# Performance work log

Hardware: AMD Instinct MI355X
Metric: run time of the kernel (lower is better)

## Reference

```python
import jax, jax.numpy as jnp
import numpy as np

G = 64      # norm_groups
T = 5       # Newton-Schulz iterations
EPS = 1e-5


def setup_inputs() -> dict:
    key = jax.random.key(0)
    weight = jax.random.normal(key, (2048, 18432), dtype=jnp.float32)
    return {"weight": weight}


def reference(weight):
    out_ch = weight.shape[0]
    # Z: [G, c, d] with c = out_ch // G, d = prod(rest)
    Z = weight.reshape(G, out_ch // G, -1)
    Zc = Z - jnp.mean(Z, axis=-1, keepdims=True)
    # S = Zc @ Zc^T : [G, c, c]
    S = jnp.einsum('gcd,ged->gce', Zc, Zc)
    c = S.shape[-1]
    eye = jnp.eye(c, dtype=S.dtype)
    S = S + EPS * eye
    # Frobenius norm per group, keepdim -> [G,1,1]
    norm_S = jnp.sqrt(jnp.sum(S * S, axis=(1, 2), keepdims=True))
    S = S / norm_S
    # Newton-Schulz: B_{t+1} = 1.5*B_t - 0.5 * B_t^3 @ S
    B = jnp.broadcast_to(eye, S.shape)
    for _ in range(T):
        B3 = jnp.matmul(jnp.matmul(B, B), B)
        B = 1.5 * B - 0.5 * jnp.matmul(B3, S)
    W = jnp.matmul(B, Zc) / jnp.sqrt(norm_S)
    return W.reshape(weight.shape)
```

## Files before the change

kernel.cpp:

```cpp
#include <hip/hip_runtime.h>

#define G 64
#define C 32
#define D 18432
#define NCH 16
#define TD (D / NCH)
#define NST (TD / 128)
#define EPS 1e-5f
#define NS_ITERS 5

typedef __attribute__((ext_vector_type(8))) short short8v;
typedef __attribute__((ext_vector_type(4))) float float4v;

__device__ __forceinline__ void split3(float x, unsigned short& h1,
                                       unsigned short& h2, unsigned short& h3) {
    unsigned int u = __float_as_uint(x);
    unsigned int m1 = u & 0xffff0000u;
    float r1 = x - __uint_as_float(m1);
    unsigned int u2 = __float_as_uint(r1);
    unsigned int m2 = u2 & 0xffff0000u;
    float r2 = r1 - __uint_as_float(m2);
    h1 = (unsigned short)(m1 >> 16);
    h2 = (unsigned short)(m2 >> 16);
    h3 = (unsigned short)(__float_as_uint(r2) >> 16);
}

__device__ __forceinline__ void split8(const float4& v0, const float4& v1,
                                       short8v& p1, short8v& p2, short8v& p3,
                                       float& rs) {
    float x[8] = {v0.x, v0.y, v0.z, v0.w, v1.x, v1.y, v1.z, v1.w};
#pragma unroll
    for (int j = 0; j < 8; ++j) {
        unsigned short h1, h2, h3;
        rs += x[j];
        split3(x[j], h1, h2, h3);
        p1[j] = (short)h1; p2[j] = (short)h2; p3[j] = (short)h3;
    }
}

#define MM6(T, A0, A1, A2, B0, B1, B2)                                        \
    T = __builtin_amdgcn_mfma_f32_16x16x32_bf16(A0, B0, T, 0, 0, 0);          \
    T = __builtin_amdgcn_mfma_f32_16x16x32_bf16(A0, B1, T, 0, 0, 0);          \
    T = __builtin_amdgcn_mfma_f32_16x16x32_bf16(A1, B0, T, 0, 0, 0);          \
    T = __builtin_amdgcn_mfma_f32_16x16x32_bf16(A1, B1, T, 0, 0, 0);          \
    T = __builtin_amdgcn_mfma_f32_16x16x32_bf16(A0, B2, T, 0, 0, 0);          \
    T = __builtin_amdgcn_mfma_f32_16x16x32_bf16(A2, B0, T, 0, 0, 0);

__global__ __launch_bounds__(256) void k1_gram(const float* __restrict__ W,
                                               float* __restrict__ psum,
                                               float* __restrict__ prow) {
    __shared__ float red[4 * 1056 + 4 * C];

    const int ch   = blockIdx.x;
    const int g    = blockIdx.y;
    const int bid  = g * NCH + ch;
    const int tid  = threadIdx.x;
    const int lane = tid & 63;
    const int wave = tid >> 6;

    const int rbase = lane & 15;
    const int koff  = (lane >> 4) * 8;

    const float* Zg = W + (size_t)g * C * D + (size_t)ch * TD;
    const float* p0 = Zg + (size_t)rbase * D + wave * 32 + koff;
    const float* p1 = p0 + (size_t)16 * D;

    float4v acc00 = (float4v)0.f, acc01 = (float4v)0.f;
    float4v acc10 = (float4v)0.f, acc11 = (float4v)0.f;
    float rs0 = 0.f, rs1 = 0.f;

    float4 c00 = *(const float4*)(p0);
    float4 c01 = *(const float4*)(p0 + 4);
    float4 c10 = *(const float4*)(p1);
    float4 c11 = *(const float4*)(p1 + 4);

#pragma unroll 1
    for (int st = 0; st < NST; ++st) {
        float4 n00, n01, n10, n11;
        if (st + 1 < NST) {
            const float* q0 = p0 + (st + 1) * 128;
            const float* q1 = p1 + (st + 1) * 128;
            n00 = *(const float4*)(q0);
            n01 = *(const float4*)(q0 + 4);
            n10 = *(const float4*)(q1);
            n11 = *(const float4*)(q1 + 4);
        }
        short8v fa0, fa1, fa2, fb0, fb1, fb2;
        split8(c00, c01, fa0, fa1, fa2, rs0);
        split8(c10, c11, fb0, fb1, fb2, rs1);

        MM6(acc00, fa0, fa1, fa2, fa0, fa1, fa2)
        MM6(acc01, fa0, fa1, fa2, fb0, fb1, fb2)
        MM6(acc10, fb0, fb1, fb2, fa0, fa1, fa2)
        MM6(acc11, fb0, fb1, fb2, fb0, fb1, fb2)

        c00 = n00; c01 = n01; c10 = n10; c11 = n11;
    }

    rs0 += __shfl_xor(rs0, 16, 64); rs0 += __shfl_xor(rs0, 32, 64);
    rs1 += __shfl_xor(rs1, 16, 64); rs1 += __shfl_xor(rs1, 32, 64);
    if (lane < 16) {
        red[4224 + wave * C + lane]      = rs0;
        red[4224 + wave * C + 16 + lane] = rs1;
    }

    {
        const int rq  = (lane >> 4) << 2;
        const int cl  = lane & 15;
        float* base = red + wave * 1056;
#pragma unroll
        for (int j = 0; j < 4; ++j) {
            base[(rq + j) * 33 + cl]            = acc00[j];
            base[(rq + j) * 33 + 16 + cl]       = acc01[j];
            base[(16 + rq + j) * 33 + cl]       = acc10[j];
            base[(16 + rq + j) * 33 + 16 + cl]  = acc11[j];
        }
    }
    __syncthreads();

#pragma unroll
    for (int k = 0; k < 4; ++k) {
        int el = tid + 256 * k;
        int row = el >> 5, col = el & 31;
        int o = row * 33 + col;
        float sv = red[o] + red[1056 + o] + red[2112 + o] + red[3168 + o];
        psum[(size_t)bid * (C * C) + el] = sv;
    }
    if (tid < C) {
        float s = red[4224 + tid] + red[4224 + C + tid] +
                  red[4224 + 2 * C + tid] + red[4224 + 3 * C + tid];
        prow[(size_t)bid * C + tid] = s;
    }
}

__global__ __launch_bounds__(256) void k2_ns(const float* __restrict__ psum,
                                             const float* __restrict__ prow,
                                             float* __restrict__ MT,
                                             float* __restrict__ vout) {
    __shared__ float S[C][C + 1];
    __shared__ float B[C][C + 1];
    __shared__ float T1[C][C + 1];
    __shared__ float T2[C][C + 1];
    __shared__ float mean[C];
    __shared__ float redw[4];
    __shared__ float normsh;

    const int g   = blockIdx.x;
    const int tid = threadIdx.x;
    const int e   = tid & 31;
    const int cbq = tid >> 5;

    float selt[4];
#pragma unroll
    for (int k = 0; k < 4; ++k) {
        int el = tid + 256 * k;
        float s = 0.f;
#pragma unroll
        for (int ch = 0; ch < NCH; ++ch)
            s += psum[((size_t)g * NCH + ch) * (C * C) + el];
        selt[k] = s;
    }
    if (tid < C) {
        float s = 0.f;
#pragma unroll
        for (int ch = 0; ch < NCH; ++ch)
            s += prow[((size_t)g * NCH + ch) * C + tid];
        mean[tid] = s / (float)D;
    }
    __syncthreads();

    float ss = 0.f;
#pragma unroll
    for (int k = 0; k < 4; ++k) {
        int el = tid + 256 * k;
        int c = el >> 5;
        float sv = selt[k] - (float)D * mean[c] * mean[e];
        if (c == e) sv += EPS;
        S[c][e] = sv;
        ss = fmaf(sv, sv, ss);
    }
#pragma unroll
    for (int off = 32; off >= 1; off >>= 1) ss += __shfl_xor(ss, off, 64);
    if ((tid & 63) == 0) redw[tid >> 6] = ss;
    __syncthreads();
    if (tid == 0) normsh = sqrtf(redw[0] + redw[1] + redw[2] + redw[3]);
    __syncthreads();
    const float inv_norm = 1.0f / normsh;
#pragma unroll
    for (int k = 0; k < 4; ++k) {
        int c = cbq + 8 * k;
        S[c][e] *= inv_norm;
        B[c][e] = (c == e) ? 1.f : 0.f;
    }
    __syncthreads();

    for (int it = 0; it < NS_ITERS; ++it) {
#pragma unroll
        for (int k = 0; k < 4; ++k) {
            int c = cbq + 8 * k;
            float s = 0.f;
            for (int kk = 0; kk < C; ++kk)
                s = fmaf(B[c][kk], B[kk][e], s);
            T1[c][e] = s;
        }
        __syncthreads();
#pragma unroll
        for (int k = 0; k < 4; ++k) {
            int c = cbq + 8 * k;
            float s = 0.f;
            for (int kk = 0; kk < C; ++kk)
                s = fmaf(T1[c][kk], B[kk][e], s);
            T2[c][e] = s;
        }
        __syncthreads();
        float pv[4];
#pragma unroll
        for (int k = 0; k < 4; ++k) {
            int c = cbq + 8 * k;
            float s = 0.f;
            for (int kk = 0; kk < C; ++kk)
                s = fmaf(T2[c][kk], S[kk][e], s);
            pv[k] = s;
        }
#pragma unroll
        for (int k = 0; k < 4; ++k) {
            int c = cbq + 8 * k;
            B[c][e] = 1.5f * B[c][e] - 0.5f * pv[k];
        }
        __syncthreads();
    }

    const float invs = 1.0f / sqrtf(normsh);
#pragma unroll
    for (int k = 0; k < 4; ++k) {
        int c = cbq + 8 * k;
        MT[(size_t)g * (C * C) + e * C + c] = B[c][e] * invs;
    }
    if (tid < C) {
        float s = 0.f;
        for (int ee = 0; ee < C; ++ee)
            s = fmaf(B[tid][ee] * invs, mean[ee], s);
        vout[(size_t)g * C + tid] = s;
    }
}

__global__ __launch_bounds__(256) void k3_apply(const float* __restrict__ W,
                                                const float* __restrict__ MT,
                                                const float* __restrict__ vv,
                                                float* __restrict__ out) {
    const int bpg = D / 1024;
    const int g   = blockIdx.x / bpg;
    const int cbk = blockIdx.x % bpg;
    const int d0  = cbk * 1024 + (int)threadIdx.x * 4;
    const float* Zg = W + (size_t)g * C * D + d0;
    const float* Mg = MT + (size_t)g * (C * C);

    float4 acc[C];
#pragma unroll
    for (int r = 0; r < C; ++r) acc[r] = make_float4(0.f, 0.f, 0.f, 0.f);

#pragma unroll 4
    for (int e = 0; e < C; ++e) {
        float4 z = *(const float4*)(Zg + (size_t)e * D);
#pragma unroll
        for (int r = 0; r < C; ++r) {
            float m = Mg[e * C + r];
            acc[r].x = fmaf(m, z.x, acc[r].x);
            acc[r].y = fmaf(m, z.y, acc[r].y);
            acc[r].z = fmaf(m, z.z, acc[r].z);
            acc[r].w = fmaf(m, z.w, acc[r].w);
        }
    }

    float* Og = out + (size_t)g * C * D + d0;
#pragma unroll
    for (int r = 0; r < C; ++r) {
        float vr = vv[g * C + r];
        float4 o = make_float4(acc[r].x - vr, acc[r].y - vr,
                               acc[r].z - vr, acc[r].w - vr);
        *(float4*)(Og + (size_t)r * D) = o;
    }
}

extern "C" void kernel_launch(void* const* d_in, const int* in_sizes, int n_in,
                              void* d_out, int out_size, void* d_ws, size_t ws_size,
                              hipStream_t stream) {
    const float* w = (const float*)d_in[0];
    float* out = (float*)d_out;

    float* psum = (float*)d_ws;
    float* prow = psum + (size_t)(G * NCH) * (C * C);
    float* MT   = prow + (size_t)(G * NCH) * C;
    float* vv   = MT   + (size_t)G * (C * C);

    k1_gram<<<dim3(NCH, G), 256, 0, stream>>>(w, psum, prow);
    k2_ns  <<<G,            256, 0, stream>>>(psum, prow, MT, vv);
    k3_apply<<<G * (D / 1024), 256, 0, stream>>>(w, MT, vv, out);
}
```

Baseline: 95.11 us.

## Fuse gram, Newton-Schulz and apply into one cooperative kernel with grid sync

Replaces the three-kernel pipeline with a single cooperative kernel of 256 blocks of 512 threads, four blocks per group. Each block computes a partial Gram over a quarter of the columns, then a grid-wide sync follows. Every block redundantly runs the Newton-Schulz iteration for its group and applies the result to its own column quarter. This removes two kernel launches and the serialized small k2 launch, and may keep W warm in cache, at the cost of a grid barrier, redundant NS work, and far fewer blocks (256) for the memory-bound apply phase. The old three-kernel path remains as a fallback if the workspace is too small or the cooperative launch fails.

After: 186.0 us. 95.6% more time.

```diff
diff --git a/kernel.cpp b/kernel.cpp
--- a/kernel.cpp
+++ b/kernel.cpp
@@ -1,13 +1,18 @@
 #include <hip/hip_runtime.h>
+#include <hip/hip_cooperative_groups.h>
+
+namespace cg = cooperative_groups;
 
 #define G 64
 #define C 32
 #define D 18432
+#define QCOLS 4608
+#define NSTEP (QCOLS / 256)
+#define EPS 1e-5f
+#define NS_ITERS 5
 #define NCH 16
 #define TD (D / NCH)
 #define NST (TD / 128)
-#define EPS 1e-5f
-#define NS_ITERS 5
 
 typedef __attribute__((ext_vector_type(8))) short short8v;
 typedef __attribute__((ext_vector_type(4))) float float4v;
@@ -46,34 +51,263 @@
     T = __builtin_amdgcn_mfma_f32_16x16x32_bf16(A0, B2, T, 0, 0, 0);          \
     T = __builtin_amdgcn_mfma_f32_16x16x32_bf16(A2, B0, T, 0, 0, 0);
 
+__global__ __launch_bounds__(512, 2) void fused_all(const float* __restrict__ W,
+                                                    float* __restrict__ psum,
+                                                    float* __restrict__ prow,
+                                                    float* __restrict__ mtb,
+                                                    float* __restrict__ vvb,
+                                                    float* __restrict__ out) {
+    __shared__ __align__(16) float red[8704];
+    __shared__ float mean[C];
+    __shared__ float redw[8];
+    __shared__ float normsh;
+
+    const int b    = blockIdx.x;
+    const int g    = b >> 2;
+    const int q    = b & 3;
+    const int tid  = threadIdx.x;
+    const int lane = tid & 63;
+    const int wave = tid >> 6;
+
+    {
+        const int rbase = lane & 15;
+        const int koff  = (lane >> 4) * 8;
+        const float* Zg = W + (size_t)g * C * D + (size_t)q * QCOLS;
+        const float* p0 = Zg + (size_t)rbase * D + wave * 32 + koff;
+        const float* p1 = p0 + (size_t)16 * D;
+
+        float4v acc00 = (float4v)0.f, acc01 = (float4v)0.f;
+        float4v acc10 = (float4v)0.f, acc11 = (float4v)0.f;
+        float rs0 = 0.f, rs1 = 0.f;
+
+        float4 c00 = *(const float4*)(p0);
+        float4 c01 = *(const float4*)(p0 + 4);
+        float4 c10 = *(const float4*)(p1);
+        float4 c11 = *(const float4*)(p1 + 4);
+
+#pragma unroll 1
+        for (int st = 0; st < NSTEP; ++st) {
+            float4 n00, n01, n10, n11;
+            if (st + 1 < NSTEP) {
+                const float* q0 = p0 + (st + 1) * 256;
+                const float* q1 = p1 + (st + 1) * 256;
+                n00 = *(const float4*)(q0);
+                n01 = *(const float4*)(q0 + 4);
+                n10 = *(const float4*)(q1);
+                n11 = *(const float4*)(q1 + 4);
+            }
+            short8v fa0, fa1, fa2, fb0, fb1, fb2;
+            split8(c00, c01, fa0, fa1, fa2, rs0);
+            split8(c10, c11, fb0, fb1, fb2, rs1);
+
+            MM6(acc00, fa0, fa1, fa2, fa0, fa1, fa2)
+            MM6(acc01, fa0, fa1, fa2, fb0, fb1, fb2)
+            MM6(acc10, fb0, fb1, fb2, fa0, fa1, fa2)
+            MM6(acc11, fb0, fb1, fb2, fb0, fb1, fb2)
+
+            c00 = n00; c01 = n01; c10 = n10; c11 = n11;
+        }
+
+        rs0 += __shfl_xor(rs0, 16, 64); rs0 += __shfl_xor(rs0, 32, 64);
+        rs1 += __shfl_xor(rs1, 16, 64); rs1 += __shfl_xor(rs1, 32, 64);
+        if (lane < 16) {
+            red[8448 + wave * 32 + lane]      = rs0;
+            red[8448 + wave * 32 + 16 + lane] = rs1;
+        }
+        {
+            const int rq = (lane >> 4) << 2;
+            const int cl = lane & 15;
+            float* base = red + wave * 1056;
+#pragma unroll
+            for (int j = 0; j < 4; ++j) {
+                base[(rq + j) * 33 + cl]           = acc00[j];
+                base[(rq + j) * 33 + 16 + cl]      = acc01[j];
+                base[(16 + rq + j) * 33 + cl]      = acc10[j];
+                base[(16 + rq + j) * 33 + 16 + cl] = acc11[j];
+            }
+        }
+        __syncthreads();
+#pragma unroll
+        for (int k = 0; k < 2; ++k) {
+            int el  = tid + 512 * k;
+            int row = el >> 5, col = el & 31;
+            int o   = row * 33 + col;
+            float sv = 0.f;
+#pragma unroll
+            for (int wv = 0; wv < 8; ++wv) sv += red[wv * 1056 + o];
+            psum[(size_t)b * 1024 + el] = sv;
+        }
+        if (tid < C) {
+            float s = 0.f;
+#pragma unroll
+            for (int wv = 0; wv < 8; ++wv) s += red[8448 + wv * 32 + tid];
+            prow[(size_t)b * 32 + tid] = s;
+        }
+    }
+
+    __threadfence();
+    cg::this_grid().sync();
+
+    {
+        const int e  = tid & 31;
+        const int cb = tid >> 5;
+        float* Sm  = red;
+        float* Bm  = red + 1056;
+        float* T1m = red + 2112;
+        float* T2m = red + 3168;
+
+        float selt0 = 0.f, selt1 = 0.f;
+#pragma unroll
+        for (int q2 = 0; q2 < 4; ++q2) {
+            const float* ps = psum + (size_t)(g * 4 + q2) * 1024;
+            selt0 += ps[tid];
+            selt1 += ps[tid + 512];
+        }
+        if (tid < C) {
+            float s = 0.f;
+#pragma unroll
+            for (int q2 = 0; q2 < 4; ++q2) s += prow[(size_t)(g * 4 + q2) * 32 + tid];
+            mean[tid] = s / (float)D;
+        }
+        __syncthreads();
+
+        float ss = 0.f;
+        {
+            int c = cb;
+            float sv = selt0 - (float)D * mean[c] * mean[e];
+            if (c == e) sv += EPS;
+            Sm[c * 33 + e] = sv; ss = fmaf(sv, sv, ss);
+            c = cb + 16;
+            sv = selt1 - (float)D * mean[c] * mean[e];
+            if (c == e) sv += EPS;
+            Sm[c * 33 + e] = sv; ss = fmaf(sv, sv, ss);
+        }
+#pragma unroll
+        for (int off = 32; off >= 1; off >>= 1) ss += __shfl_xor(ss, off, 64);
+        if (lane == 0) redw[wave] = ss;
+        __syncthreads();
+        if (tid == 0) {
+            float t = 0.f;
+#pragma unroll
+            for (int wv = 0; wv < 8; ++wv) t += redw[wv];
+            normsh = sqrtf(t);
+        }
+        __syncthreads();
+        const float inv_norm = 1.0f / normsh;
+#pragma unroll
+        for (int k = 0; k < 2; ++k) {
+            int c = cb + 16 * k;
+            Sm[c * 33 + e] *= inv_norm;
+            Bm[c * 33 + e] = (c == e) ? 1.f : 0.f;
+        }
+        __syncthreads();
+
+        for (int it = 0; it < NS_ITERS; ++it) {
+#pragma unroll
+            for (int k = 0; k < 2; ++k) {
+                int c = cb + 16 * k;
+                float s = 0.f;
+                for (int kk = 0; kk < C; ++kk)
+                    s = fmaf(Bm[c * 33 + kk], Bm[kk * 33 + e], s);
+                T1m[c * 33 + e] = s;
+            }
+            __syncthreads();
+#pragma unroll
+            for (int k = 0; k < 2; ++k) {
+                int c = cb + 16 * k;
+                float s = 0.f;
+                for (int kk = 0; kk < C; ++kk)
+                    s = fmaf(T1m[c * 33 + kk], Bm[kk * 33 + e], s);
+                T2m[c * 33 + e] = s;
+            }
+            __syncthreads();
+            float pv0 = 0.f, pv1 = 0.f;
+            for (int kk = 0; kk < C; ++kk)
+                pv0 = fmaf(T2m[cb * 33 + kk], Sm[kk * 33 + e], pv0);
+            for (int kk = 0; kk < C; ++kk)
+                pv1 = fmaf(T2m[(cb + 16) * 33 + kk], Sm[kk * 33 + e], pv1);
+            Bm[cb * 33 + e]        = 1.5f * Bm[cb * 33 + e] - 0.5f * pv0;
+            Bm[(cb + 16) * 33 + e] = 1.5f * Bm[(cb + 16) * 33 + e] - 0.5f * pv1;
+            __syncthreads();
+        }
+
+        const float invs = 1.0f / sqrtf(normsh);
+#pragma unroll
+        for (int k = 0; k < 2; ++k) {
+            int c = cb + 16 * k;
+            mtb[(size_t)b * 1024 + e * C + c] = Bm[c * 33 + e] * invs;
+        }
+        if (tid < C) {
+            float s = 0.f;
+            for (int ee = 0; ee < C; ++ee)
+                s = fmaf(Bm[tid * 33 + ee] * invs, mean[ee], s);
+            vvb[(size_t)b * 32 + tid] = s;
+        }
+    }
+    __syncthreads();
+
+    {
+        const float* Mg = mtb + (size_t)b * 1024;
+        const float* vg = vvb + (size_t)b * 32;
+        const float* Zb = W + (size_t)g * C * D;
+        float*       Ob = out + (size_t)g * C * D;
+
+#pragma unroll 1
+        for (int p = 0; p < 3; ++p) {
+            int u = tid + p * 512;
+            if (u < 1152) {
+                const int c4 = q * 1152 + u;
+                const float* Zc = Zb + (size_t)c4 * 4;
+                float4 acc[C];
+#pragma unroll
+                for (int r = 0; r < C; ++r) acc[r] = make_float4(0.f, 0.f, 0.f, 0.f);
+#pragma unroll 4
+                for (int e2 = 0; e2 < C; ++e2) {
+                    float4 z = *(const float4*)(Zc + (size_t)e2 * D);
+#pragma unroll
+                    for (int r = 0; r < C; ++r) {
+                        float m = Mg[e2 * C + r];
+                        acc[r].x = fmaf(m, z.x, acc[r].x);
+                        acc[r].y = fmaf(m, z.y, acc[r].y);
+                        acc[r].z = fmaf(m, z.z, acc[r].z);
+                        acc[r].w = fmaf(m, z.w, acc[r].w);
+                    }
+                }
+                float* Oc = Ob + (size_t)c4 * 4;
+#pragma unroll
+                for (int r = 0; r < C; ++r) {
+                    float vr = vg[r];
+                    float4 o = make_float4(acc[r].x - vr, acc[r].y - vr,
+                                           acc[r].z - vr, acc[r].w - vr);
+                    *(float4*)(Oc + (size_t)r * D) = o;
+                }
+            }
+        }
+    }
+}
+
 __global__ __launch_bounds__(256) void k1_gram(const float* __restrict__ W,
                                                float* __restrict__ psum,
                                                float* __restrict__ prow) {
     __shared__ float red[4 * 1056 + 4 * C];
-
     const int ch   = blockIdx.x;
     const int g    = blockIdx.y;
     const int bid  = g * NCH + ch;
     const int tid  = threadIdx.x;
     const int lane = tid & 63;
     const int wave = tid >> 6;
-
     const int rbase = lane & 15;
     const int koff  = (lane >> 4) * 8;
-
     const float* Zg = W + (size_t)g * C * D + (size_t)ch * TD;
     const float* p0 = Zg + (size_t)rbase * D + wave * 32 + koff;
     const float* p1 = p0 + (size_t)16 * D;
-
     float4v acc00 = (float4v)0.f, acc01 = (float4v)0.f;
     float4v acc10 = (float4v)0.f, acc11 = (float4v)0.f;
     float rs0 = 0.f, rs1 = 0.f;
-
     float4 c00 = *(const float4*)(p0);
     float4 c01 = *(const float4*)(p0 + 4);
     float4 c10 = *(const float4*)(p1);
     float4 c11 = *(const float4*)(p1 + 4);
-
 #pragma unroll 1
     for (int st = 0; st < NST; ++st) {
         float4 n00, n01, n10, n11;
@@ -88,36 +322,31 @@
         short8v fa0, fa1, fa2, fb0, fb1, fb2;
         split8(c00, c01, fa0, fa1, fa2, rs0);
         split8(c10, c11, fb0, fb1, fb2, rs1);
-
         MM6(acc00, fa0, fa1, fa2, fa0, fa1, fa2)
         MM6(acc01, fa0, fa1, fa2, fb0, fb1, fb2)
         MM6(acc10, fb0, fb1, fb2, fa0, fa1, fa2)
         MM6(acc11, fb0, fb1, fb2, fb0, fb1, fb2)
-
         c00 = n00; c01 = n01; c10 = n10; c11 = n11;
     }
-
     rs0 += __shfl_xor(rs0, 16, 64); rs0 += __shfl_xor(rs0, 32, 64);
     rs1 += __shfl_xor(rs1, 16, 64); rs1 += __shfl_xor(rs1, 32, 64);
     if (lane < 16) {
         red[4224 + wave * C + lane]      = rs0;
         red[4224 + wave * C + 16 + lane] = rs1;
     }
-
     {
-        const int rq  = (lane >> 4) << 2;
-        const int cl  = lane & 15;
+        const int rq = (lane >> 4) << 2;
+        const int cl = lane & 15;
         float* base = red + wave * 1056;
 #pragma unroll
         for (int j = 0; j < 4; ++j) {
-            base[(rq + j) * 33 + cl]            = acc00[j];
-            base[(rq + j) * 33 + 16 + cl]       = acc01[j];
-            base[(16 + rq + j) * 33 + cl]       = acc10[j];
-            base[(16 + rq + j) * 33 + 16 + cl]  = acc11[j];
+            base[(rq + j) * 33 + cl]           = acc00[j];
+            base[(rq + j) * 33 + 16 + cl]      = acc01[j];
+            base[(16 + rq + j) * 33 + cl]      = acc10[j];
+            base[(16 + rq + j) * 33 + 16 + cl] = acc11[j];
         }
     }
     __syncthreads();
-
 #pragma unroll
     for (int k = 0; k < 4; ++k) {
         int el = tid + 256 * k;
@@ -144,12 +373,10 @@
     __shared__ float mean[C];
     __shared__ float redw[4];
     __shared__ float normsh;
-
     const int g   = blockIdx.x;
     const int tid = threadIdx.x;
     const int e   = tid & 31;
     const int cbq = tid >> 5;
-
     float selt[4];
 #pragma unroll
     for (int k = 0; k < 4; ++k) {
@@ -168,7 +395,6 @@
         mean[tid] = s / (float)D;
     }
     __syncthreads();
-
     float ss = 0.f;
 #pragma unroll
     for (int k = 0; k < 4; ++k) {
@@ -193,7 +419,6 @@
         B[c][e] = (c == e) ? 1.f : 0.f;
     }
     __syncthreads();
-
     for (int it = 0; it < NS_ITERS; ++it) {
 #pragma unroll
         for (int k = 0; k < 4; ++k) {
@@ -229,7 +454,6 @@
         }
         __syncthreads();
     }
-
     const float invs = 1.0f / sqrtf(normsh);
 #pragma unroll
     for (int k = 0; k < 4; ++k) {
@@ -254,11 +478,9 @@
     const int d0  = cbk * 1024 + (int)threadIdx.x * 4;
     const float* Zg = W + (size_t)g * C * D + d0;
     const float* Mg = MT + (size_t)g * (C * C);
-
     float4 acc[C];
 #pragma unroll
     for (int r = 0; r < C; ++r) acc[r] = make_float4(0.f, 0.f, 0.f, 0.f);
-
 #pragma unroll 4
     for (int e = 0; e < C; ++e) {
         float4 z = *(const float4*)(Zg + (size_t)e * D);
@@ -271,7 +493,6 @@
             acc[r].w = fmaf(m, z.w, acc[r].w);
         }
     }
-
     float* Og = out + (size_t)g * C * D + d0;
 #pragma unroll
     for (int r = 0; r < C; ++r) {
@@ -288,12 +509,26 @@
     const float* w = (const float*)d_in[0];
     float* out = (float*)d_out;
 
-    float* psum = (float*)d_ws;
-    float* prow = psum + (size_t)(G * NCH) * (C * C);
-    float* MT   = prow + (size_t)(G * NCH) * C;
-    float* vv   = MT   + (size_t)G * (C * C);
-
-    k1_gram<<<dim3(NCH, G), 256, 0, stream>>>(w, psum, prow);
-    k2_ns  <<<G,            256, 0, stream>>>(psum, prow, MT, vv);
-    k3_apply<<<G * (D / 1024), 256, 0, stream>>>(w, MT, vv, out);
-}
+    const size_t fused_need = (size_t)(256 * 1024 + 256 * 32) * 2 * sizeof(float);
+    bool done = false;
+    if (ws_size >= fused_need) {
+        float* psum = (float*)d_ws;
+        float* prow = psum + 256 * 1024;
+        float* mtb  = prow + 256 * 32;
+        float* vvb  = mtb + 256 * 1024;
+        void* args[] = {(void*)&w, (void*)&psum, (void*)&prow,
+                        (void*)&mtb, (void*)&vvb, (void*)&out};
+        hipError_t err = hipLaunchCooperativeKernel((void*)fused_all, dim3(256),
+                                                    dim3(512), args, 0, stream);
+        done = (err == hipSuccess);
+    }
+    if (!done) {
+        float* psum = (float*)d_ws;
+        float* prow = psum + (size_t)(G * NCH) * (C * C);
+        float* MT   = prow + (size_t)(G * NCH) * C;
+        float* vv   = MT + (size_t)G * (C * C);
+        k1_gram<<<dim3(NCH, G), 256, 0, stream>>>(w, psum, prow);
+        k2_ns<<<G, 256, 0, stream>>>(psum, prow, MT, vv);
+        k3_apply<<<G * (D / 1024), 256, 0, stream>>>(w, MT, vv, out);
+    }
+}
```
